# Optimization experiments

Hardware: AMD Instinct MI355X
Metric: run time of the kernel (lower is better)

## Reference

```python
import jax, jax.numpy as jnp
import numpy as np

N_EMBD = 1024
N_HEAD = 16
HEAD_SIZE = N_EMBD // N_HEAD  # 64
ROPE_BASE = 10000.0


def apply_rope(x, pos):
    # x: [B, T, H, D] (torchtune layout), interleaved-pair rotation
    D = x.shape[-1]
    theta = 1.0 / (ROPE_BASE ** (jnp.arange(0, D, 2, dtype=jnp.float32) / D))  # [D/2]
    ang = pos.astype(jnp.float32)[:, None] * theta[None, :]                    # [T, D/2]
    cos = jnp.cos(ang)[None, :, None, :].astype(x.dtype)
    sin = jnp.sin(ang)[None, :, None, :].astype(x.dtype)
    xr = x.reshape(*x.shape[:-1], D // 2, 2)
    x0, x1 = xr[..., 0], xr[..., 1]
    out = jnp.stack([x0 * cos - x1 * sin, x1 * cos + x0 * sin], axis=-1)
    return out.reshape(x.shape)


def setup_inputs() -> dict:
    key = jax.random.key(0)
    k1, k2, k3 = jax.random.split(key, 3)
    B, T = 4, 1000
    x = jax.random.normal(k1, (B, T, N_EMBD), dtype=jnp.float32)
    # causal boolean mask (True = attend), as passed to F.scaled_dot_product_attention
    attn_mask = jnp.tril(jnp.ones((T, T), dtype=bool))[None, None, :, :]
    # Linear weights stored as [in, out] (i.e. torch weight transposed), fan-in scaled
    W_attn = jax.random.normal(k2, (N_EMBD, 3 * N_EMBD), dtype=jnp.float32) * (1.0 / np.sqrt(N_EMBD))
    W_proj = jax.random.normal(k3, (N_EMBD, N_EMBD), dtype=jnp.float32) * (1.0 / np.sqrt(N_EMBD))
    return {"x": x, "attn_mask": attn_mask, "W_attn": W_attn, "W_proj": W_proj}


def reference(x, attn_mask, W_attn, W_proj):
    B, T, C = x.shape
    qkv = x @ W_attn                                   # [B, T, 3C]
    q, k, v = jnp.split(qkv, 3, axis=-1)
    q = q.reshape(B, T, N_HEAD, HEAD_SIZE)
    k = k.reshape(B, T, N_HEAD, HEAD_SIZE)
    v = v.reshape(B, T, N_HEAD, HEAD_SIZE)
    pos = jnp.arange(T)
    q = apply_rope(q, pos)
    k = apply_rope(k, pos)
    # causal SDPA (dropout = 0)
    scale = 1.0 / np.sqrt(HEAD_SIZE)
    scores = jnp.einsum('bqhd,bkhd->bhqk', q, k) * scale   # [B, H, T, T]
    neg = jnp.asarray(jnp.finfo(scores.dtype).min, scores.dtype)
    scores = jnp.where(attn_mask, scores, neg)
    probs = jax.nn.softmax(scores, axis=-1)
    y = jnp.einsum('bhqk,bkhd->bqhd', probs, v)             # [B, T, H, D]
    y = y.reshape(B, T, C)
    return y @ W_proj
```

## Files before the change

### kernel.cpp

```cpp
#include <hip/hip_runtime.h>

typedef unsigned short ushortT;
typedef unsigned int uintT;
typedef __attribute__((ext_vector_type(8))) short bf16x8;
typedef __attribute__((ext_vector_type(4))) float f32x4;

#define B_ 4
#define T_ 1000
#define H_ 16
#define MP 4096
#define QSCALE 0.18033688011112042f

__device__ __forceinline__ ushortT f2bf(float f) {
    unsigned u = __float_as_uint(f);
    u += 0x7fffu + ((u >> 16) & 1u);
    return (ushortT)(u >> 16);
}
__device__ __forceinline__ float fast_exp2(float x) {
#if __has_builtin(__builtin_amdgcn_exp2f)
    return __builtin_amdgcn_exp2f(x);
#else
    return exp2f(x);
#endif
}

__global__ void prep_kernel(const float* __restrict__ x,
                            const float* __restrict__ Wa, const float* __restrict__ Wp,
                            ushortT* __restrict__ Xb,
                            ushortT* __restrict__ Wat, ushortT* __restrict__ Wpt) {
    __shared__ float tile[64][65];
    int bid = blockIdx.x, tid = threadIdx.x;
    if (bid < 4096) {
        int e = (bid * 256 + tid) * 4;
        int r = e >> 10, col = e & 1023;
        int b = r >> 10, t = r & 1023;
        ushort4 o = make_ushort4(0, 0, 0, 0);
        if (t < T_) {
            float4 v = *(const float4*)(x + (((size_t)(b * T_ + t)) << 10) + col);
            o.x = f2bf(v.x); o.y = f2bf(v.y); o.z = f2bf(v.z); o.w = f2bf(v.w);
        }
        *(ushort4*)(Xb + (size_t)e) = o;
        return;
    }
    const float* W; ushortT* Wt; int N, bx, by;
    if (bid < 4096 + 768) { W = Wa; Wt = Wat; N = 3072; int id = bid - 4096; bx = id % 48; by = id / 48; }
    else                  { W = Wp; Wt = Wpt; N = 1024; int id = bid - 4864; bx = id & 15; by = id >> 4; }
    int k0 = by * 64, n0 = bx * 64;
    int lane = tid & 63, w4 = tid >> 6;
#pragma unroll 4
    for (int i = 0; i < 16; ++i) {
        int row = i * 4 + w4;
        tile[row][lane] = W[(size_t)(k0 + row) * N + n0 + lane];
    }
    __syncthreads();
#pragma unroll 4
    for (int i = 0; i < 16; ++i) {
        int row = i * 4 + w4;
        Wt[(size_t)(n0 + row) * 1024 + k0 + lane] = f2bf(tile[lane][row]);
    }
}

__global__ __launch_bounds__(256, 2) void gemm_qkv_kernel(
    const ushortT* __restrict__ A, const ushortT* __restrict__ Bt,
    ushortT* __restrict__ Qb, ushortT* __restrict__ Kb, ushortT* __restrict__ Vtb)
{
    __shared__ __align__(16) ushortT smem[16896];
    ushortT* As = smem;
    ushortT* Bs = smem + 8192;
    const int K = 1024;
    int tid = threadIdx.x, wave = tid >> 6, lane = tid & 63;
    int m0 = blockIdx.y * 128, n0 = blockIdx.x * 128;
    int wm = (wave >> 1) * 64, wn = (wave & 1) * 64;
    int col0 = lane & 15, quad = lane >> 4;

    f32x4 acc[4][4] = {};

    for (int kt = 0; kt < 16; ++kt) {
        int k0 = kt * 64;
        __syncthreads();
#pragma unroll
        for (int it = 0; it < 4; ++it) {
            int gci = (wave * 4 + it) * 64 + lane;
            int r = gci >> 3, c = gci & 7;
            int sc = c ^ (r & 7);
            const ushortT* ga = A + (size_t)(m0 + r) * K + k0 + sc * 8;
            __builtin_amdgcn_global_load_lds(
                (const __attribute__((address_space(1))) unsigned int*)ga,
                (__attribute__((address_space(3))) unsigned int*)(As + (wave * 4 + it) * 512),
                16, 0, 0);
            const ushortT* gb = Bt + (size_t)(n0 + r) * K + k0 + sc * 8;
            __builtin_amdgcn_global_load_lds(
                (const __attribute__((address_space(1))) unsigned int*)gb,
                (__attribute__((address_space(3))) unsigned int*)(Bs + (wave * 4 + it) * 512),
                16, 0, 0);
        }
        __syncthreads();
#pragma unroll
        for (int s = 0; s < 2; ++s) {
            int g = s * 4 + quad;
            bf16x8 af[4], bfr[4];
#pragma unroll
            for (int mi = 0; mi < 4; ++mi) {
                int r = wm + mi * 16 + col0;
                af[mi] = *(const bf16x8*)(As + r * 64 + ((g ^ (r & 7)) * 8));
            }
#pragma unroll
            for (int ni = 0; ni < 4; ++ni) {
                int r = wn + ni * 16 + col0;
                bfr[ni] = *(const bf16x8*)(Bs + r * 64 + ((g ^ (r & 7)) * 8));
            }
#pragma unroll
            for (int mi = 0; mi < 4; ++mi)
#pragma unroll
                for (int ni = 0; ni < 4; ++ni)
                    acc[mi][ni] = __builtin_amdgcn_mfma_f32_16x16x32_bf16(
                        af[mi], bfr[ni], acc[mi][ni], 0, 0, 0);
        }
    }
    __syncthreads();

    int sec = n0 >> 10, cb = n0 & 1023;
    int b = m0 >> 10, tbase = m0 & 1023;

    if (sec < 2) {
        float2* tab = (float2*)smem;
#pragma unroll
        for (int i = 0; i < 16; ++i) {
            int task = i * 256 + tid;
            int tl = task >> 5, p = task & 31;
            float theta = __expf(-(float)p * 0.28782313662425572f);
            float ang = (float)(tbase + tl) * theta;
            float sn, cs;
            sincosf(ang, &sn, &cs);
            tab[tl * 33 + p] = make_float2(cs, sn);
        }
        __syncthreads();
        ushortT* Out = sec ? Kb : Qb;
        float qs = sec ? 1.0f : QSCALE;
#pragma unroll
        for (int mi = 0; mi < 4; ++mi) {
#pragma unroll
            for (int j = 0; j < 4; ++j) {
                int tl = wm + mi * 16 + quad * 4 + j;
                int t = tbase + tl;
                bool valid = t < T_;
#pragma unroll
                for (int nt = 0; nt < 4; ++nt) {
                    float xv = acc[mi][nt][j];
                    float xp = __shfl_xor(xv, 1);
                    int cl = wn + nt * 16 + col0;
                    int d = cl & 63;
                    float2 cssn = tab[tl * 33 + (d >> 1)];
                    float r = (d & 1) ? (xv * cssn.x + xp * cssn.y)
                                      : (xv * cssn.x - xp * cssn.y);
                    r *= qs;
                    if (valid)
                        Out[((size_t)((b << 4) | ((cb + cl) >> 6)) << 16) + (t << 6) + d] = f2bf(r);
                }
            }
        }
    } else {
        ushortT* Ls = smem;
#pragma unroll
        for (int mi = 0; mi < 4; ++mi) {
#pragma unroll
            for (int nt = 0; nt < 4; ++nt) {
                int cl = wn + nt * 16 + col0;
                int rb = wm + mi * 16 + quad * 4;
                uintT lo = (uintT)f2bf(acc[mi][nt][0]) | ((uintT)f2bf(acc[mi][nt][1]) << 16);
                uintT hi = (uintT)f2bf(acc[mi][nt][2]) | ((uintT)f2bf(acc[mi][nt][3]) << 16);
                *(uint2*)(Ls + cl * 132 + rb) = make_uint2(lo, hi);
            }
        }
        __syncthreads();
#pragma unroll
        for (int it = 0; it < 8; ++it) {
            int u = it * 256 + tid;
            int cl = u >> 4, c = u & 15;
            int d = cl & 63, h = (cb + cl) >> 6;
            ushortT tmp[8];
#pragma unroll
            for (int j = 0; j < 8; ++j) tmp[j] = Ls[cl * 132 + j * 16 + c];
            *(bf16x8*)(Vtb + (((size_t)((b << 4) | h)) << 16) + ((size_t)d << 10) + tbase + c * 8)
                = *(bf16x8*)tmp;
        }
    }
}

#define PSTR 136
template <bool LAST>
__device__ __forceinline__ void softmax_store(f32x4* sc4, ushortT* Ps,
                                              int wave, int quad, int col0,
                                              int q0, int j0) {
#pragma unroll
    for (int reg = 0; reg < 4; ++reg) {
        int m = quad * 4 + reg;
        int q = q0 + wave * 16 + m;
        float pv[8];
#pragma unroll
        for (int nt = 0; nt < 8; ++nt) {
            float p = fast_exp2(sc4[nt][reg]);
            if (LAST && (j0 + nt * 16 + col0) > q) p = 0.f;
            pv[nt] = p;
        }
        int4 pk;
        pk.x = __builtin_amdgcn_perm(__float_as_uint(pv[1]), __float_as_uint(pv[0]), 0x07060302u);
        pk.y = __builtin_amdgcn_perm(__float_as_uint(pv[3]), __float_as_uint(pv[2]), 0x07060302u);
        pk.z = __builtin_amdgcn_perm(__float_as_uint(pv[5]), __float_as_uint(pv[4]), 0x07060302u);
        pk.w = __builtin_amdgcn_perm(__float_as_uint(pv[7]), __float_as_uint(pv[6]), 0x07060302u);
        *(int4*)(Ps + (wave * 16 + m) * PSTR + col0 * 8) = pk;
    }
}

__global__ __launch_bounds__(256, 3) void attn_mfma_kernel(
    const ushortT* __restrict__ Qb, const ushortT* __restrict__ Kb,
    const ushortT* __restrict__ Vtb, ushortT* __restrict__ Yb)
{
    __shared__ __align__(16) ushortT Ks[128 * 64];
    __shared__ __align__(16) ushortT Vs[64 * 128];
    __shared__ __align__(16) ushortT Ps[64 * PSTR];

    int flat = blockIdx.y * 64 + blockIdx.x;
    int xcd = flat & 7;
    int slot = flat >> 3;
    int bh = xcd * 8 + (slot & 7);
    int qi = 15 - (slot >> 3);
    int b = bh >> 4, h = bh & 15;
    int q0 = qi * 64;
    int tid = threadIdx.x, wave = tid >> 6, lane = tid & 63;
    int col0 = lane & 15, quad = lane >> 4;

    const ushortT* Kbh  = Kb  + ((size_t)bh << 16);
    const ushortT* Vtbh = Vtb + ((size_t)bh << 16);

    const ushortT* qrowp = Qb + ((size_t)bh << 16) + (size_t)(q0 + wave * 16 + col0) * 64;
    bf16x8 aq[2];
    aq[0] = *(const bf16x8*)(qrowp + quad * 8);
    aq[1] = *(const bf16x8*)(qrowp + 32 + quad * 8);

    bf16x8 onesb;
#pragma unroll
    for (int i = 0; i < 8; ++i) onesb[i] = (short)0x3F80;

    f32x4 o[4] = {};
    f32x4 lsum = {};

    int nchunks = qi / 2 + 1;
    for (int cc = 0; cc < nchunks; ++cc) {
        int j0 = cc * 128;
        __syncthreads();
#pragma unroll
        for (int it = 0; it < 4; ++it) {
            int gci = (wave * 4 + it) * 64 + lane;
            {
                int r = gci >> 3, c = gci & 7;
                int sc = c ^ (r & 7);
                const ushortT* gk = Kbh + (size_t)(j0 + r) * 64 + sc * 8;
                __builtin_amdgcn_global_load_lds(
                    (const __attribute__((address_space(1))) unsigned int*)gk,
                    (__attribute__((address_space(3))) unsigned int*)(Ks + (wave * 4 + it) * 512),
                    16, 0, 0);
            }
            {
                int d = gci >> 4, c = gci & 15;
                int sc = c ^ (d & 15);
                const ushortT* gv = Vtbh + (size_t)d * 1024 + j0 + sc * 8;
                __builtin_amdgcn_global_load_lds(
                    (const __attribute__((address_space(1))) unsigned int*)gv,
                    (__attribute__((address_space(3))) unsigned int*)(Vs + (wave * 4 + it) * 512),
                    16, 0, 0);
            }
        }
        __syncthreads();

        f32x4 sc4[8] = {};
#pragma unroll
        for (int s = 0; s < 2; ++s) {
#pragma unroll
            for (int nt = 0; nt < 8; ++nt) {
                int r = nt * 16 + col0;
                bf16x8 bk = *(const bf16x8*)(Ks + r * 64 + (((s * 4 + quad) ^ (col0 & 7)) * 8));
                sc4[nt] = __builtin_amdgcn_mfma_f32_16x16x32_bf16(aq[s], bk, sc4[nt], 0, 0, 0);
            }
        }

        if (cc == nchunks - 1)
            softmax_store<true>(sc4, Ps, wave, quad, col0, q0, j0);
        else
            softmax_store<false>(sc4, Ps, wave, quad, col0, q0, j0);

#pragma unroll
        for (int s = 0; s < 4; ++s) {
            bf16x8 ap = *(const bf16x8*)(Ps + (wave * 16 + col0) * PSTR + s * 32 + quad * 8);
            lsum = __builtin_amdgcn_mfma_f32_16x16x32_bf16(ap, onesb, lsum, 0, 0, 0);
#pragma unroll
            for (int nt = 0; nt < 4; ++nt) {
                int d = nt * 16 + col0;
                bf16x8 bv = *(const bf16x8*)(Vs + d * 128 + (((s * 4 + quad) ^ col0) * 8));
                o[nt] = __builtin_amdgcn_mfma_f32_16x16x32_bf16(ap, bv, o[nt], 0, 0, 0);
            }
        }
    }

#pragma unroll
    for (int reg = 0; reg < 4; ++reg) {
        int q = q0 + wave * 16 + quad * 4 + reg;
        if (q < T_) {
            float inv_l = 1.0f / lsum[reg];
            ushortT* yp = Yb + ((size_t)(b * 1024 + q) << 10) + h * 64;
#pragma unroll
            for (int nt = 0; nt < 4; ++nt)
                yp[nt * 16 + col0] = f2bf(o[nt][reg] * inv_l);
        }
    }
}

__global__ __launch_bounds__(256, 3) void gemm_proj_kernel(
    const ushortT* __restrict__ A, const ushortT* __restrict__ Bt,
    float* __restrict__ Cout)
{
    __shared__ __align__(16) ushortT As[64 * 64];
    __shared__ __align__(16) ushortT Bs[128 * 64];
    const int K = 1024;
    int tid = threadIdx.x, wave = tid >> 6, lane = tid & 63;
    int m0 = blockIdx.y * 64, n0 = blockIdx.x * 128;
    int wm = (wave >> 1) * 32, wn = (wave & 1) * 64;
    int col0 = lane & 15, quad = lane >> 4;

    f32x4 acc[2][4] = {};

    for (int kt = 0; kt < 16; ++kt) {
        int k0 = kt * 64;
        __syncthreads();
#pragma unroll
        for (int it = 0; it < 2; ++it) {
            int gci = it * 256 + tid;
            int r = gci >> 3, c = gci & 7;
            int sc = c ^ (r & 7);
            const ushortT* ga = A + (size_t)(m0 + r) * K + k0 + sc * 8;
            __builtin_amdgcn_global_load_lds(
                (const __attribute__((address_space(1))) unsigned int*)ga,
                (__attribute__((address_space(3))) unsigned int*)(As + it * 2048 + wave * 512),
                16, 0, 0);
        }
#pragma unroll
        for (int it = 0; it < 4; ++it) {
            int gci = it * 256 + tid;
            int r = gci >> 3, c = gci & 7;
            int sc = c ^ (r & 7);
            const ushortT* gb = Bt + (size_t)(n0 + r) * K + k0 + sc * 8;
            __builtin_amdgcn_global_load_lds(
                (const __attribute__((address_space(1))) unsigned int*)gb,
                (__attribute__((address_space(3))) unsigned int*)(Bs + it * 2048 + wave * 512),
                16, 0, 0);
        }
        __syncthreads();
#pragma unroll
        for (int s = 0; s < 2; ++s) {
            int g = s * 4 + quad;
            bf16x8 af[2], bfr[4];
#pragma unroll
            for (int mi = 0; mi < 2; ++mi) {
                int r = wm + mi * 16 + col0;
                af[mi] = *(const bf16x8*)(As + r * 64 + ((g ^ (r & 7)) * 8));
            }
#pragma unroll
            for (int ni = 0; ni < 4; ++ni) {
                int r = wn + ni * 16 + col0;
                bfr[ni] = *(const bf16x8*)(Bs + r * 64 + ((g ^ (r & 7)) * 8));
            }
#pragma unroll
            for (int mi = 0; mi < 2; ++mi)
#pragma unroll
                for (int ni = 0; ni < 4; ++ni)
                    acc[mi][ni] = __builtin_amdgcn_mfma_f32_16x16x32_bf16(
                        af[mi], bfr[ni], acc[mi][ni], 0, 0, 0);
        }
    }

#pragma unroll
    for (int mi = 0; mi < 2; ++mi) {
#pragma unroll
        for (int j = 0; j < 4; ++j) {
            int row = m0 + wm + mi * 16 + quad * 4 + j;
            int t = row & 1023, b = row >> 10;
            if (t < T_) {
                float* cp = Cout + ((size_t)(b * T_ + t) << 10) + n0 + wn;
#pragma unroll
                for (int ni = 0; ni < 4; ++ni)
                    cp[ni * 16 + col0] = acc[mi][ni][j];
            }
        }
    }
}

extern "C" void kernel_launch(void* const* d_in, const int* in_sizes, int n_in,
                              void* d_out, int out_size, void* d_ws, size_t ws_size,
                              hipStream_t stream) {
    const float* x      = (const float*)d_in[0];
    const float* W_attn = (const float*)d_in[2];
    const float* W_proj = (const float*)d_in[3];
    float* out = (float*)d_out;

    uintptr_t w = (uintptr_t)d_ws;
    ushortT* Xb  = (ushortT*)(w);
    ushortT* Wat = (ushortT*)(w + 8388608);
    ushortT* Wpt = (ushortT*)(w + 14680064);
    ushortT* Qb  = (ushortT*)(w + 16777216);
    ushortT* Kb  = (ushortT*)(w + 25165824);
    ushortT* Vtb = (ushortT*)(w + 33554432);
    ushortT* Yb  = (ushortT*)(w + 41943040);

    prep_kernel<<<dim3(5120), dim3(256), 0, stream>>>(x, W_attn, W_proj, Xb, Wat, Wpt);

    gemm_qkv_kernel<<<dim3(24, 32), dim3(256), 0, stream>>>(Xb, Wat, Qb, Kb, Vtb);

    attn_mfma_kernel<<<dim3(64, 16), dim3(256), 0, stream>>>(Qb, Kb, Vtb, Yb);

    gemm_proj_kernel<<<dim3(8, 64), dim3(256), 0, stream>>>(Yb, Wpt, out);
}
```

Baseline: 151.4 us.

## Split long causal attention tiles across two blocks and combine partials

```diff
diff --git a/kernel.cpp b/kernel.cpp
--- a/kernel.cpp
+++ b/kernel.cpp
@@ -214,19 +214,25 @@
 
 __global__ __launch_bounds__(256, 3) void attn_mfma_kernel(
     const ushortT* __restrict__ Qb, const ushortT* __restrict__ Kb,
-    const ushortT* __restrict__ Vtb, ushortT* __restrict__ Yb)
+    const ushortT* __restrict__ Vtb, ushortT* __restrict__ Yb,
+    float* __restrict__ Opart)
 {
     __shared__ __align__(16) ushortT Ks[128 * 64];
     __shared__ __align__(16) ushortT Vs[64 * 128];
     __shared__ __align__(16) ushortT Ps[64 * PSTR];
 
-    int flat = blockIdx.y * 64 + blockIdx.x;
+    int flat = blockIdx.x;
     int xcd = flat & 7;
     int slot = flat >> 3;
-    int bh = xcd * 8 + (slot & 7);
-    int qi = 15 - (slot >> 3);
+    int bhl = slot & 7;
+    int widx = slot >> 3;
+    int bh = xcd * 8 + bhl;
+    int qi, sp, S;
+    if (widx < 16) { qi = 15 - (widx >> 1); sp = widx & 1; S = 2; }
+    else           { qi = 7 - (widx - 16); sp = 0; S = 1; }
     int b = bh >> 4, h = bh & 15;
     int q0 = qi * 64;
+    int nchunks = qi / 2 + 1;
     int tid = threadIdx.x, wave = tid >> 6, lane = tid & 63;
     int col0 = lane & 15, quad = lane >> 4;
 
@@ -245,8 +251,7 @@
     f32x4 o[4] = {};
     f32x4 lsum = {};
 
-    int nchunks = qi / 2 + 1;
-    for (int cc = 0; cc < nchunks; ++cc) {
+    for (int cc = sp; cc < nchunks; cc += S) {
         int j0 = cc * 128;
         __syncthreads();
 #pragma unroll
@@ -302,17 +307,61 @@
         }
     }
 
-#pragma unroll
-    for (int reg = 0; reg < 4; ++reg) {
-        int q = q0 + wave * 16 + quad * 4 + reg;
-        if (q < T_) {
+    if (S == 1) {
+#pragma unroll
+        for (int reg = 0; reg < 4; ++reg) {
+            int q = q0 + wave * 16 + quad * 4 + reg;
             float inv_l = 1.0f / lsum[reg];
             ushortT* yp = Yb + ((size_t)(b * 1024 + q) << 10) + h * 64;
 #pragma unroll
             for (int nt = 0; nt < 4; ++nt)
                 yp[nt * 16 + col0] = f2bf(o[nt][reg] * inv_l);
         }
-    }
+    } else {
+        int part_id = bh * 16 + (15 - qi) * 2 + sp;
+        float* Op = Opart + (size_t)part_id * 4160;
+#pragma unroll
+        for (int reg = 0; reg < 4; ++reg) {
+            int qr = wave * 16 + quad * 4 + reg;
+#pragma unroll
+            for (int nt = 0; nt < 4; ++nt)
+                Op[qr * 64 + nt * 16 + col0] = o[nt][reg];
+            if (col0 == 0)
+                Op[4096 + qr] = lsum[reg];
+        }
+    }
+}
+
+__global__ __launch_bounds__(256) void combine_kernel(
+    const float* __restrict__ Opart, ushortT* __restrict__ Yb)
+{
+    int flat = blockIdx.x;
+    int xcd = flat & 7;
+    int bhl = (flat >> 3) & 7;
+    int qidx = flat >> 6;
+    int bh = xcd * 8 + bhl;
+    int qi = 15 - qidx;
+    int b = bh >> 4, h = bh & 15;
+    const float* P0 = Opart + (size_t)(bh * 16 + qidx * 2) * 4160;
+    const float* P1 = P0 + 4160;
+    int tid = threadIdx.x;
+    int q = tid >> 2, dg = (tid & 3) * 16;
+    int tg = qi * 64 + q;
+    if (tg >= T_) return;
+    float inv = 1.0f / (P0[4096 + q] + P1[4096 + q]);
+    ushortT outv[16];
+#pragma unroll
+    for (int i = 0; i < 4; ++i) {
+        float4 a = *(const float4*)(P0 + q * 64 + dg + i * 4);
+        float4 c = *(const float4*)(P1 + q * 64 + dg + i * 4);
+        outv[i * 4 + 0] = f2bf((a.x + c.x) * inv);
+        outv[i * 4 + 1] = f2bf((a.y + c.y) * inv);
+        outv[i * 4 + 2] = f2bf((a.z + c.z) * inv);
+        outv[i * 4 + 3] = f2bf((a.w + c.w) * inv);
+    }
+    ushortT* yp = Yb + ((size_t)(b * 1024 + tg) << 10) + h * 64 + dg;
+    *(bf16x8*)yp = *(bf16x8*)outv;
+    *(bf16x8*)(yp + 8) = *(bf16x8*)(outv + 8);
 }
 
 __global__ __launch_bounds__(256, 3) void gemm_proj_kernel(
@@ -403,19 +452,22 @@
     float* out = (float*)d_out;
 
     uintptr_t w = (uintptr_t)d_ws;
-    ushortT* Xb  = (ushortT*)(w);
-    ushortT* Wat = (ushortT*)(w + 8388608);
-    ushortT* Wpt = (ushortT*)(w + 14680064);
-    ushortT* Qb  = (ushortT*)(w + 16777216);
-    ushortT* Kb  = (ushortT*)(w + 25165824);
-    ushortT* Vtb = (ushortT*)(w + 33554432);
-    ushortT* Yb  = (ushortT*)(w + 41943040);
+    ushortT* Xb    = (ushortT*)(w);
+    ushortT* Wat   = (ushortT*)(w + 8388608);
+    ushortT* Wpt   = (ushortT*)(w + 14680064);
+    ushortT* Qb    = (ushortT*)(w + 16777216);
+    ushortT* Kb    = (ushortT*)(w + 25165824);
+    ushortT* Vtb   = (ushortT*)(w + 33554432);
+    ushortT* Yb    = (ushortT*)(w + 41943040);
+    float*   Opart = (float*)(w + 50331648);
 
     prep_kernel<<<dim3(5120), dim3(256), 0, stream>>>(x, W_attn, W_proj, Xb, Wat, Wpt);
 
     gemm_qkv_kernel<<<dim3(24, 32), dim3(256), 0, stream>>>(Xb, Wat, Qb, Kb, Vtb);
 
-    attn_mfma_kernel<<<dim3(64, 16), dim3(256), 0, stream>>>(Qb, Kb, Vtb, Yb);
+    attn_mfma_kernel<<<dim3(1536), dim3(256), 0, stream>>>(Qb, Kb, Vtb, Yb, Opart);
+
+    combine_kernel<<<dim3(512), dim3(256), 0, stream>>>(Opart, Yb);
 
     gemm_proj_kernel<<<dim3(8, 64), dim3(256), 0, stream>>>(Yb, Wpt, out);
 }
```

Result: slower. 161.1 us (+6.5%).

## Double-buffer 64-wide K/V tiles in attention with prefetch of next chunk

Applied to the files above, without the earlier changes.

```diff
diff --git a/kernel.cpp b/kernel.cpp
--- a/kernel.cpp
+++ b/kernel.cpp
@@ -174,50 +174,28 @@
         }
         __syncthreads();
 #pragma unroll
-        for (int it = 0; it < 8; ++it) {
+        for (int it = 0; it < 16; ++it) {
             int u = it * 256 + tid;
-            int cl = u >> 4, c = u & 15;
+            int c4 = u & 15;
+            int g  = (u >> 4) & 1;
+            int cl = u >> 5;
             int d = cl & 63, h = (cb + cl) >> 6;
-            ushortT tmp[8];
-#pragma unroll
-            for (int j = 0; j < 8; ++j) tmp[j] = Ls[cl * 132 + j * 16 + c];
-            *(bf16x8*)(Vtb + (((size_t)((b << 4) | h)) << 16) + ((size_t)d << 10) + tbase + c * 8)
-                = *(bf16x8*)tmp;
-        }
-    }
-}
-
-#define PSTR 136
-template <bool LAST>
-__device__ __forceinline__ void softmax_store(f32x4* sc4, ushortT* Ps,
-                                              int wave, int quad, int col0,
-                                              int q0, int j0) {
-#pragma unroll
-    for (int reg = 0; reg < 4; ++reg) {
-        int m = quad * 4 + reg;
-        int q = q0 + wave * 16 + m;
-        float pv[8];
-#pragma unroll
-        for (int nt = 0; nt < 8; ++nt) {
-            float p = fast_exp2(sc4[nt][reg]);
-            if (LAST && (j0 + nt * 16 + col0) > q) p = 0.f;
-            pv[nt] = p;
-        }
-        int4 pk;
-        pk.x = __builtin_amdgcn_perm(__float_as_uint(pv[1]), __float_as_uint(pv[0]), 0x07060302u);
-        pk.y = __builtin_amdgcn_perm(__float_as_uint(pv[3]), __float_as_uint(pv[2]), 0x07060302u);
-        pk.z = __builtin_amdgcn_perm(__float_as_uint(pv[5]), __float_as_uint(pv[4]), 0x07060302u);
-        pk.w = __builtin_amdgcn_perm(__float_as_uint(pv[7]), __float_as_uint(pv[6]), 0x07060302u);
-        *(int4*)(Ps + (wave * 16 + m) * PSTR + col0 * 8) = pk;
-    }
-}
-
+            ushortT tmp[4];
+#pragma unroll
+            for (int j = 0; j < 4; ++j) tmp[j] = Ls[cl * 132 + g * 64 + j * 16 + c4];
+            *(uint2*)(Vtb + (((size_t)((b << 4) | h)) << 16) + ((size_t)d << 10)
+                      + tbase + g * 64 + c4 * 4) = *(uint2*)tmp;
+        }
+    }
+}
+
+#define PSTR 68
 __global__ __launch_bounds__(256, 3) void attn_mfma_kernel(
     const ushortT* __restrict__ Qb, const ushortT* __restrict__ Kb,
     const ushortT* __restrict__ Vtb, ushortT* __restrict__ Yb)
 {
-    __shared__ __align__(16) ushortT Ks[128 * 64];
-    __shared__ __align__(16) ushortT Vs[64 * 128];
+    __shared__ __align__(16) ushortT Ks[2][64 * 64];
+    __shared__ __align__(16) ushortT Vs[2][64 * 64];
     __shared__ __align__(16) ushortT Ps[64 * PSTR];
 
     int flat = blockIdx.y * 64 + blockIdx.x;
@@ -245,58 +223,75 @@
     f32x4 o[4] = {};
     f32x4 lsum = {};
 
-    int nchunks = qi / 2 + 1;
+    int nchunks = qi + 1;
+
+    auto stage = [&](int cc, ushortT* KsB, ushortT* VsB) {
+#pragma unroll
+        for (int it = 0; it < 2; ++it) {
+            int gci = (wave * 2 + it) * 64 + lane;
+            int r = gci >> 3, c = gci & 7;
+            int sc = c ^ (r & 7);
+            const ushortT* gk = Kbh + (size_t)(cc * 64 + r) * 64 + sc * 8;
+            __builtin_amdgcn_global_load_lds(
+                (const __attribute__((address_space(1))) unsigned int*)gk,
+                (__attribute__((address_space(3))) unsigned int*)(KsB + (wave * 2 + it) * 512),
+                16, 0, 0);
+            const ushortT* gv = Vtbh + (size_t)r * 1024 + cc * 64 + sc * 8;
+            __builtin_amdgcn_global_load_lds(
+                (const __attribute__((address_space(1))) unsigned int*)gv,
+                (__attribute__((address_space(3))) unsigned int*)(VsB + (wave * 2 + it) * 512),
+                16, 0, 0);
+        }
+    };
+
+    stage(0, Ks[0], Vs[0]);
+
     for (int cc = 0; cc < nchunks; ++cc) {
-        int j0 = cc * 128;
-        __syncthreads();
-#pragma unroll
-        for (int it = 0; it < 4; ++it) {
-            int gci = (wave * 4 + it) * 64 + lane;
-            {
-                int r = gci >> 3, c = gci & 7;
-                int sc = c ^ (r & 7);
-                const ushortT* gk = Kbh + (size_t)(j0 + r) * 64 + sc * 8;
-                __builtin_amdgcn_global_load_lds(
-                    (const __attribute__((address_space(1))) unsigned int*)gk,
-                    (__attribute__((address_space(3))) unsigned int*)(Ks + (wave * 4 + it) * 512),
-                    16, 0, 0);
-            }
-            {
-                int d = gci >> 4, c = gci & 15;
-                int sc = c ^ (d & 15);
-                const ushortT* gv = Vtbh + (size_t)d * 1024 + j0 + sc * 8;
-                __builtin_amdgcn_global_load_lds(
-                    (const __attribute__((address_space(1))) unsigned int*)gv,
-                    (__attribute__((address_space(3))) unsigned int*)(Vs + (wave * 4 + it) * 512),
-                    16, 0, 0);
-            }
-        }
-        __syncthreads();
-
-        f32x4 sc4[8] = {};
+        __syncthreads();
+        if (cc + 1 < nchunks)
+            stage(cc + 1, Ks[(cc + 1) & 1], Vs[(cc + 1) & 1]);
+
+        const ushortT* KsC = Ks[cc & 1];
+        const ushortT* VsC = Vs[cc & 1];
+        int j0 = cc * 64;
+
+        f32x4 sc4[4] = {};
 #pragma unroll
         for (int s = 0; s < 2; ++s) {
 #pragma unroll
-            for (int nt = 0; nt < 8; ++nt) {
+            for (int nt = 0; nt < 4; ++nt) {
                 int r = nt * 16 + col0;
-                bf16x8 bk = *(const bf16x8*)(Ks + r * 64 + (((s * 4 + quad) ^ (col0 & 7)) * 8));
+                bf16x8 bk = *(const bf16x8*)(KsC + r * 64 + (((s * 4 + quad) ^ (r & 7)) * 8));
                 sc4[nt] = __builtin_amdgcn_mfma_f32_16x16x32_bf16(aq[s], bk, sc4[nt], 0, 0, 0);
             }
         }
 
-        if (cc == nchunks - 1)
-            softmax_store<true>(sc4, Ps, wave, quad, col0, q0, j0);
-        else
-            softmax_store<false>(sc4, Ps, wave, quad, col0, q0, j0);
-
-#pragma unroll
-        for (int s = 0; s < 4; ++s) {
+        bool last = (cc == nchunks - 1);
+#pragma unroll
+        for (int reg = 0; reg < 4; ++reg) {
+            int m = quad * 4 + reg;
+            int q = q0 + wave * 16 + m;
+            float pv[4];
+#pragma unroll
+            for (int nt = 0; nt < 4; ++nt) {
+                float p = fast_exp2(sc4[nt][reg]);
+                if (last && (j0 + nt * 16 + col0) > q) p = 0.f;
+                pv[nt] = p;
+            }
+            uint2 pk;
+            pk.x = __builtin_amdgcn_perm(__float_as_uint(pv[1]), __float_as_uint(pv[0]), 0x07060302u);
+            pk.y = __builtin_amdgcn_perm(__float_as_uint(pv[3]), __float_as_uint(pv[2]), 0x07060302u);
+            *(uint2*)(Ps + (wave * 16 + m) * PSTR + col0 * 4) = pk;
+        }
+
+#pragma unroll
+        for (int s = 0; s < 2; ++s) {
             bf16x8 ap = *(const bf16x8*)(Ps + (wave * 16 + col0) * PSTR + s * 32 + quad * 8);
             lsum = __builtin_amdgcn_mfma_f32_16x16x32_bf16(ap, onesb, lsum, 0, 0, 0);
 #pragma unroll
             for (int nt = 0; nt < 4; ++nt) {
                 int d = nt * 16 + col0;
-                bf16x8 bv = *(const bf16x8*)(Vs + d * 128 + (((s * 4 + quad) ^ col0) * 8));
+                bf16x8 bv = *(const bf16x8*)(VsC + d * 64 + (((s * 4 + quad) ^ (d & 7)) * 8));
                 o[nt] = __builtin_amdgcn_mfma_f32_16x16x32_bf16(ap, bv, o[nt], 0, 0, 0);
             }
         }
```

Measured after the change: 156.0 us. 1.03x slower.

## Fuse prep, QKV GEMM, attention and projection into one cooperative persistent kernel

Applied to the files above, without the earlier changes.

```diff
diff --git a/kernel.cpp b/kernel.cpp
--- a/kernel.cpp
+++ b/kernel.cpp
@@ -1,15 +1,16 @@
 #include <hip/hip_runtime.h>
+#include <hip/hip_cooperative_groups.h>
+
+namespace cg = cooperative_groups;
 
 typedef unsigned short ushortT;
 typedef unsigned int uintT;
 typedef __attribute__((ext_vector_type(8))) short bf16x8;
 typedef __attribute__((ext_vector_type(4))) float f32x4;
 
-#define B_ 4
 #define T_ 1000
-#define H_ 16
-#define MP 4096
 #define QSCALE 0.18033688011112042f
+#define PSTR 136
 
 __device__ __forceinline__ ushortT f2bf(float f) {
     unsigned u = __float_as_uint(f);
@@ -24,382 +25,377 @@
 #endif
 }
 
-__global__ void prep_kernel(const float* __restrict__ x,
-                            const float* __restrict__ Wa, const float* __restrict__ Wp,
-                            ushortT* __restrict__ Xb,
-                            ushortT* __restrict__ Wat, ushortT* __restrict__ Wpt) {
-    __shared__ float tile[64][65];
-    int bid = blockIdx.x, tid = threadIdx.x;
-    if (bid < 4096) {
-        int e = (bid * 256 + tid) * 4;
-        int r = e >> 10, col = e & 1023;
-        int b = r >> 10, t = r & 1023;
-        ushort4 o = make_ushort4(0, 0, 0, 0);
-        if (t < T_) {
-            float4 v = *(const float4*)(x + (((size_t)(b * T_ + t)) << 10) + col);
-            o.x = f2bf(v.x); o.y = f2bf(v.y); o.z = f2bf(v.z); o.w = f2bf(v.w);
-        }
-        *(ushort4*)(Xb + (size_t)e) = o;
-        return;
-    }
-    const float* W; ushortT* Wt; int N, bx, by;
-    if (bid < 4096 + 768) { W = Wa; Wt = Wat; N = 3072; int id = bid - 4096; bx = id % 48; by = id / 48; }
-    else                  { W = Wp; Wt = Wpt; N = 1024; int id = bid - 4864; bx = id & 15; by = id >> 4; }
-    int k0 = by * 64, n0 = bx * 64;
-    int lane = tid & 63, w4 = tid >> 6;
+__global__ __launch_bounds__(256, 3) void fused_kernel(
+    const float* __restrict__ x, const float* __restrict__ Wa, const float* __restrict__ Wp,
+    ushortT* __restrict__ Xb, ushortT* __restrict__ Wat, ushortT* __restrict__ Wpt,
+    ushortT* __restrict__ Qb, ushortT* __restrict__ Kb, ushortT* __restrict__ Vtb,
+    ushortT* __restrict__ Yb, float* __restrict__ out)
+{
+    __shared__ __align__(16) ushortT smem[25088];
+    cg::grid_group grid = cg::this_grid();
+    int blk = blockIdx.x, nb = gridDim.x, tid = threadIdx.x;
+    int wave = tid >> 6, lane = tid & 63;
+    int col0 = lane & 15, quad = lane >> 4;
+
+    {
+        float (*tile)[65] = (float(*)[65])smem;
+        for (int u = blk; u < 5120; u += nb) {
+            if (u < 4096) {
+                int e = (u * 256 + tid) * 4;
+                int r = e >> 10, col = e & 1023;
+                int b = r >> 10, t = r & 1023;
+                ushort4 o = make_ushort4(0, 0, 0, 0);
+                if (t < T_) {
+                    float4 v = *(const float4*)(x + (((size_t)(b * T_ + t)) << 10) + col);
+                    o.x = f2bf(v.x); o.y = f2bf(v.y); o.z = f2bf(v.z); o.w = f2bf(v.w);
+                }
+                *(ushort4*)(Xb + (size_t)e) = o;
+            } else {
+                const float* W; ushortT* Wt; int N, bx, by;
+                int id = u - 4096;
+                if (id < 768) { W = Wa; Wt = Wat; N = 3072; bx = id % 48; by = id / 48; }
+                else          { W = Wp; Wt = Wpt; N = 1024; id -= 768; bx = id & 15; by = id >> 4; }
+                int k0 = by * 64, n0 = bx * 64;
+                int w4 = tid >> 6;
+                __syncthreads();
 #pragma unroll 4
-    for (int i = 0; i < 16; ++i) {
-        int row = i * 4 + w4;
-        tile[row][lane] = W[(size_t)(k0 + row) * N + n0 + lane];
-    }
-    __syncthreads();
+                for (int i = 0; i < 16; ++i) {
+                    int row = i * 4 + w4;
+                    tile[row][lane] = W[(size_t)(k0 + row) * N + n0 + lane];
+                }
+                __syncthreads();
 #pragma unroll 4
-    for (int i = 0; i < 16; ++i) {
-        int row = i * 4 + w4;
-        Wt[(size_t)(n0 + row) * 1024 + k0 + lane] = f2bf(tile[lane][row]);
-    }
-}
-
-__global__ __launch_bounds__(256, 2) void gemm_qkv_kernel(
-    const ushortT* __restrict__ A, const ushortT* __restrict__ Bt,
-    ushortT* __restrict__ Qb, ushortT* __restrict__ Kb, ushortT* __restrict__ Vtb)
-{
-    __shared__ __align__(16) ushortT smem[16896];
-    ushortT* As = smem;
-    ushortT* Bs = smem + 8192;
-    const int K = 1024;
-    int tid = threadIdx.x, wave = tid >> 6, lane = tid & 63;
-    int m0 = blockIdx.y * 128, n0 = blockIdx.x * 128;
-    int wm = (wave >> 1) * 64, wn = (wave & 1) * 64;
-    int col0 = lane & 15, quad = lane >> 4;
-
-    f32x4 acc[4][4] = {};
-
-    for (int kt = 0; kt < 16; ++kt) {
-        int k0 = kt * 64;
-        __syncthreads();
-#pragma unroll
-        for (int it = 0; it < 4; ++it) {
-            int gci = (wave * 4 + it) * 64 + lane;
-            int r = gci >> 3, c = gci & 7;
-            int sc = c ^ (r & 7);
-            const ushortT* ga = A + (size_t)(m0 + r) * K + k0 + sc * 8;
-            __builtin_amdgcn_global_load_lds(
-                (const __attribute__((address_space(1))) unsigned int*)ga,
-                (__attribute__((address_space(3))) unsigned int*)(As + (wave * 4 + it) * 512),
-                16, 0, 0);
-            const ushortT* gb = Bt + (size_t)(n0 + r) * K + k0 + sc * 8;
-            __builtin_amdgcn_global_load_lds(
-                (const __attribute__((address_space(1))) unsigned int*)gb,
-                (__attribute__((address_space(3))) unsigned int*)(Bs + (wave * 4 + it) * 512),
-                16, 0, 0);
-        }
-        __syncthreads();
-#pragma unroll
-        for (int s = 0; s < 2; ++s) {
-            int g = s * 4 + quad;
-            bf16x8 af[4], bfr[4];
-#pragma unroll
-            for (int mi = 0; mi < 4; ++mi) {
-                int r = wm + mi * 16 + col0;
-                af[mi] = *(const bf16x8*)(As + r * 64 + ((g ^ (r & 7)) * 8));
-            }
-#pragma unroll
-            for (int ni = 0; ni < 4; ++ni) {
-                int r = wn + ni * 16 + col0;
-                bfr[ni] = *(const bf16x8*)(Bs + r * 64 + ((g ^ (r & 7)) * 8));
-            }
-#pragma unroll
-            for (int mi = 0; mi < 4; ++mi)
-#pragma unroll
-                for (int ni = 0; ni < 4; ++ni)
-                    acc[mi][ni] = __builtin_amdgcn_mfma_f32_16x16x32_bf16(
-                        af[mi], bfr[ni], acc[mi][ni], 0, 0, 0);
+                for (int i = 0; i < 16; ++i) {
+                    int row = i * 4 + w4;
+                    Wt[(size_t)(n0 + row) * 1024 + k0 + lane] = f2bf(tile[lane][row]);
+                }
+            }
         }
     }
-    __syncthreads();
-
-    int sec = n0 >> 10, cb = n0 & 1023;
-    int b = m0 >> 10, tbase = m0 & 1023;
-
-    if (sec < 2) {
-        float2* tab = (float2*)smem;
-#pragma unroll
-        for (int i = 0; i < 16; ++i) {
-            int task = i * 256 + tid;
-            int tl = task >> 5, p = task & 31;
-            float theta = __expf(-(float)p * 0.28782313662425572f);
-            float ang = (float)(tbase + tl) * theta;
-            float sn, cs;
-            sincosf(ang, &sn, &cs);
-            tab[tl * 33 + p] = make_float2(cs, sn);
+    grid.sync();
+
+    {
+        ushortT* As = smem;
+        ushortT* Bs = smem + 8192;
+        const int K = 1024;
+        for (int tix = blk; tix < 768; tix += nb) {
+            int m0 = (tix / 24) * 128, n0 = (tix % 24) * 128;
+            int wm = (wave >> 1) * 64, wn = (wave & 1) * 64;
+
+            f32x4 acc[4][4] = {};
+
+            for (int kt = 0; kt < 16; ++kt) {
+                int k0 = kt * 64;
+                __syncthreads();
+#pragma unroll
+                for (int it = 0; it < 4; ++it) {
+                    int gci = (wave * 4 + it) * 64 + lane;
+                    int r = gci >> 3, c = gci & 7;
+                    int sc = c ^ (r & 7);
+                    const ushortT* ga = Xb + (size_t)(m0 + r) * K + k0 + sc * 8;
+                    __builtin_amdgcn_global_load_lds(
+                        (const __attribute__((address_space(1))) unsigned int*)ga,
+                        (__attribute__((address_space(3))) unsigned int*)(As + (wave * 4 + it) * 512),
+                        16, 0, 0);
+                    const ushortT* gb = Wat + (size_t)(n0 + r) * K + k0 + sc * 8;
+                    __builtin_amdgcn_global_load_lds(
+                        (const __attribute__((address_space(1))) unsigned int*)gb,
+                        (__attribute__((address_space(3))) unsigned int*)(Bs + (wave * 4 + it) * 512),
+                        16, 0, 0);
+                }
+                __syncthreads();
+#pragma unroll
+                for (int s = 0; s < 2; ++s) {
+                    int g = s * 4 + quad;
+                    bf16x8 af[4], bfr[4];
+#pragma unroll
+                    for (int mi = 0; mi < 4; ++mi) {
+                        int r = wm + mi * 16 + col0;
+                        af[mi] = *(const bf16x8*)(As + r * 64 + ((g ^ (r & 7)) * 8));
+                    }
+#pragma unroll
+                    for (int ni = 0; ni < 4; ++ni) {
+                        int r = wn + ni * 16 + col0;
+                        bfr[ni] = *(const bf16x8*)(Bs + r * 64 + ((g ^ (r & 7)) * 8));
+                    }
+#pragma unroll
+                    for (int mi = 0; mi < 4; ++mi)
+#pragma unroll
+                        for (int ni = 0; ni < 4; ++ni)
+                            acc[mi][ni] = __builtin_amdgcn_mfma_f32_16x16x32_bf16(
+                                af[mi], bfr[ni], acc[mi][ni], 0, 0, 0);
+                }
+            }
+            __syncthreads();
+
+            int sec = n0 >> 10, cb = n0 & 1023;
+            int b = m0 >> 10, tbase = m0 & 1023;
+
+            if (sec < 2) {
+                float2* tab = (float2*)smem;
+#pragma unroll
+                for (int i = 0; i < 16; ++i) {
+                    int task = i * 256 + tid;
+                    int tl = task >> 5, p = task & 31;
+                    float theta = __expf(-(float)p * 0.28782313662425572f);
+                    float ang = (float)(tbase + tl) * theta;
+                    float sn, cs;
+                    sincosf(ang, &sn, &cs);
+                    tab[tl * 33 + p] = make_float2(cs, sn);
+                }
+                __syncthreads();
+                ushortT* Out = sec ? Kb : Qb;
+                float qs = sec ? 1.0f : QSCALE;
+#pragma unroll
+                for (int mi = 0; mi < 4; ++mi) {
+#pragma unroll
+                    for (int j = 0; j < 4; ++j) {
+                        int tl = wm + mi * 16 + quad * 4 + j;
+                        int t = tbase + tl;
+                        bool valid = t < T_;
+#pragma unroll
+                        for (int nt = 0; nt < 4; ++nt) {
+                            float xv = acc[mi][nt][j];
+                            float xp = __shfl_xor(xv, 1);
+                            int cl = wn + nt * 16 + col0;
+                            int d = cl & 63;
+                            float2 cssn = tab[tl * 33 + (d >> 1)];
+                            float r = (d & 1) ? (xv * cssn.x + xp * cssn.y)
+                                              : (xv * cssn.x - xp * cssn.y);
+                            r *= qs;
+                            if (valid)
+                                Out[((size_t)((b << 4) | ((cb + cl) >> 6)) << 16) + (t << 6) + d] = f2bf(r);
+                        }
+                    }
+                }
+            } else {
+                ushortT* Ls = smem;
+#pragma unroll
+                for (int mi = 0; mi < 4; ++mi) {
+#pragma unroll
+                    for (int nt = 0; nt < 4; ++nt) {
+                        int cl = wn + nt * 16 + col0;
+                        int rb = wm + mi * 16 + quad * 4;
+                        uintT lo = (uintT)f2bf(acc[mi][nt][0]) | ((uintT)f2bf(acc[mi][nt][1]) << 16);
+                        uintT hi = (uintT)f2bf(acc[mi][nt][2]) | ((uintT)f2bf(acc[mi][nt][3]) << 16);
+                        *(uint2*)(Ls + cl * 132 + rb) = make_uint2(lo, hi);
+                    }
+                }
+                __syncthreads();
+#pragma unroll
+                for (int it = 0; it < 8; ++it) {
+                    int u = it * 256 + tid;
+                    int cl = u >> 4, c = u & 15;
+                    int d = cl & 63, h = (cb + cl) >> 6;
+                    ushortT tmp[8];
+#pragma unroll
+                    for (int j = 0; j < 8; ++j) tmp[j] = Ls[cl * 132 + j * 16 + c];
+                    *(bf16x8*)(Vtb + (((size_t)((b << 4) | h)) << 16) + ((size_t)d << 10) + tbase + c * 8)
+                        = *(bf16x8*)tmp;
+                }
+            }
         }
-        __syncthreads();
-        ushortT* Out = sec ? Kb : Qb;
-        float qs = sec ? 1.0f : QSCALE;
-#pragma unroll
-        for (int mi = 0; mi < 4; ++mi) {
-#pragma unroll
-            for (int j = 0; j < 4; ++j) {
-                int tl = wm + mi * 16 + quad * 4 + j;
-                int t = tbase + tl;
-                bool valid = t < T_;
-#pragma unroll
-                for (int nt = 0; nt < 4; ++nt) {
-                    float xv = acc[mi][nt][j];
-                    float xp = __shfl_xor(xv, 1);
-                    int cl = wn + nt * 16 + col0;
-                    int d = cl & 63;
-                    float2 cssn = tab[tl * 33 + (d >> 1)];
-                    float r = (d & 1) ? (xv * cssn.x + xp * cssn.y)
-                                      : (xv * cssn.x - xp * cssn.y);
-                    r *= qs;
-                    if (valid)
-                        Out[((size_t)((b << 4) | ((cb + cl) >> 6)) << 16) + (t << 6) + d] = f2bf(r);
+    }
+    grid.sync();
+
+    {
+        ushortT* Ks = smem;
+        ushortT* Vs = smem + 8192;
+        ushortT* Ps = smem + 16384;
+        for (int w = blk; w < 1024; w += nb) {
+            int xcd = w & 7;
+            int slot = w >> 3;
+            int bh = xcd * 8 + (slot & 7);
+            int qi = 15 - (slot >> 3);
+            int b = bh >> 4, h = bh & 15;
+            int q0 = qi * 64;
+
+            const ushortT* Kbh  = Kb  + ((size_t)bh << 16);
+            const ushortT* Vtbh = Vtb + ((size_t)bh << 16);
+
+            const ushortT* qrowp = Qb + ((size_t)bh << 16) + (size_t)(q0 + wave * 16 + col0) * 64;
+            bf16x8 aq[2];
+            aq[0] = *(const bf16x8*)(qrowp + quad * 8);
+            aq[1] = *(const bf16x8*)(qrowp + 32 + quad * 8);
+
+            bf16x8 onesb;
+#pragma unroll
+            for (int i = 0; i < 8; ++i) onesb[i] = (short)0x3F80;
+
+            f32x4 o[4] = {};
+            f32x4 lsum = {};
+
+            int nchunks = qi / 2 + 1;
+            for (int cc = 0; cc < nchunks; ++cc) {
+                int j0 = cc * 128;
+                __syncthreads();
+#pragma unroll
+                for (int it = 0; it < 4; ++it) {
+                    int gci = (wave * 4 + it) * 64 + lane;
+                    {
+                        int r = gci >> 3, c = gci & 7;
+                        int sc = c ^ (r & 7);
+                        const ushortT* gk = Kbh + (size_t)(j0 + r) * 64 + sc * 8;
+                        __builtin_amdgcn_global_load_lds(
+                            (const __attribute__((address_space(1))) unsigned int*)gk,
+                            (__attribute__((address_space(3))) unsigned int*)(Ks + (wave * 4 + it) * 512),
+                            16, 0, 0);
+                    }
+                    {
+                        int d = gci >> 4, c = gci & 15;
+                        int sc = c ^ (d & 15);
+                        const ushortT* gv = Vtbh + (size_t)d * 1024 + j0 + sc * 8;
+                        __builtin_amdgcn_global_load_lds(
+                            (const __attribute__((address_space(1))) unsigned int*)gv,
+                            (__attribute__((address_space(3))) unsigned int*)(Vs + (wave * 4 + it) * 512),
+                            16, 0, 0);
+                    }
+                }
+                __syncthreads();
+
+                f32x4 sc4[8] = {};
+#pragma unroll
+                for (int s = 0; s < 2; ++s) {
+#pragma unroll
+                    for (int nt = 0; nt < 8; ++nt) {
+                        int r = nt * 16 + col0;
+                        bf16x8 bk = *(const bf16x8*)(Ks + r * 64 + (((s * 4 + quad) ^ (col0 & 7)) * 8));
+                        sc4[nt] = __builtin_amdgcn_mfma_f32_16x16x32_bf16(aq[s], bk, sc4[nt], 0, 0, 0);
+                    }
+                }
+
+                bool last = (cc == nchunks - 1);
+#pragma unroll
+                for (int reg = 0; reg < 4; ++reg) {
+                    int m = quad * 4 + reg;
+                    int q = q0 + wave * 16 + m;
+                    float pv[8];
+#pragma unroll
+                    for (int nt = 0; nt < 8; ++nt) {
+                        float p = fast_exp2(sc4[nt][reg]);
+                        if (last && (j0 + nt * 16 + col0) > q) p = 0.f;
+                        pv[nt] = p;
+                    }
+                    int4 pk;
+                    pk.x = __builtin_amdgcn_perm(__float_as_uint(pv[1]), __float_as_uint(pv[0]), 0x07060302u);
+                    pk.y = __builtin_amdgcn_perm(__float_as_uint(pv[3]), __float_as_uint(pv[2]), 0x07060302u);
+                    pk.z = __builtin_amdgcn_perm(__float_as_uint(pv[5]), __float_as_uint(pv[4]), 0x07060302u);
+                    pk.w = __builtin_amdgcn_perm(__float_as_uint(pv[7]), __float_as_uint(pv[6]), 0x07060302u);
+                    *(int4*)(Ps + (wave * 16 + m) * PSTR + col0 * 8) = pk;
+                }
+
+#pragma unroll
+                for (int s = 0; s < 4; ++s) {
+                    bf16x8 ap = *(const bf16x8*)(Ps + (wave * 16 + col0) * PSTR + s * 32 + quad * 8);
+                    lsum = __builtin_amdgcn_mfma_f32_16x16x32_bf16(ap, onesb, lsum, 0, 0, 0);
+#pragma unroll
+                    for (int nt = 0; nt < 4; ++nt) {
+                        int d = nt * 16 + col0;
+                        bf16x8 bv = *(const bf16x8*)(Vs + d * 128 + (((s * 4 + quad) ^ col0) * 8));
+                        o[nt] = __builtin_amdgcn_mfma_f32_16x16x32_bf16(ap, bv, o[nt], 0, 0, 0);
+                    }
+                }
+            }
+
+#pragma unroll
+            for (int reg = 0; reg < 4; ++reg) {
+                int q = q0 + wave * 16 + quad * 4 + reg;
+                if (q < T_) {
+                    float inv_l = 1.0f / lsum[reg];
+                    ushortT* yp = Yb + ((size_t)(b * 1024 + q) << 10) + h * 64;
+#pragma unroll
+                    for (int nt = 0; nt < 4; ++nt)
+                        yp[nt * 16 + col0] = f2bf(o[nt][reg] * inv_l);
                 }
             }
         }
-    } else {
-        ushortT* Ls = smem;
-#pragma unroll
-        for (int mi = 0; mi < 4; ++mi) {
-#pragma unroll
-            for (int nt = 0; nt < 4; ++nt) {
-                int cl = wn + nt * 16 + col0;
-                int rb = wm + mi * 16 + quad * 4;
-                uintT lo = (uintT)f2bf(acc[mi][nt][0]) | ((uintT)f2bf(acc[mi][nt][1]) << 16);
-                uintT hi = (uintT)f2bf(acc[mi][nt][2]) | ((uintT)f2bf(acc[mi][nt][3]) << 16);
-                *(uint2*)(Ls + cl * 132 + rb) = make_uint2(lo, hi);
-            }
-        }
-        __syncthreads();
-#pragma unroll
-        for (int it = 0; it < 8; ++it) {
-            int u = it * 256 + tid;
-            int cl = u >> 4, c = u & 15;
-            int d = cl & 63, h = (cb + cl) >> 6;
-            ushortT tmp[8];
-#pragma unroll
-            for (int j = 0; j < 8; ++j) tmp[j] = Ls[cl * 132 + j * 16 + c];
-            *(bf16x8*)(Vtb + (((size_t)((b << 4) | h)) << 16) + ((size_t)d << 10) + tbase + c * 8)
-                = *(bf16x8*)tmp;
+    }
+    grid.sync();
+
+    {
+        ushortT* As = smem;
+        ushortT* Bs = smem + 4096;
+        const int K = 1024;
+        for (int w = blk; w < 512; w += nb) {
+            int m0 = (w >> 3) * 64, n0 = (w & 7) * 128;
+            int wm = (wave >> 1) * 32, wn = (wave & 1) * 64;
+
+            f32x4 acc[2][4] = {};
+
+            for (int kt = 0; kt < 16; ++kt) {
+                int k0 = kt * 64;
+                __syncthreads();
+#pragma unroll
+                for (int it = 0; it < 2; ++it) {
+                    int gci = it * 256 + tid;
+                    int r = gci >> 3, c = gci & 7;
+                    int sc = c ^ (r & 7);
+                    const ushortT* ga = Yb + (size_t)(m0 + r) * K + k0 + sc * 8;
+                    __builtin_amdgcn_global_load_lds(
+                        (const __attribute__((address_space(1))) unsigned int*)ga,
+                        (__attribute__((address_space(3))) unsigned int*)(As + it * 2048 + wave * 512),
+                        16, 0, 0);
+                }
+#pragma unroll
+                for (int it = 0; it < 4; ++it) {
+                    int gci = it * 256 + tid;
+                    int r = gci >> 3, c = gci & 7;
+                    int sc = c ^ (r & 7);
+                    const ushortT* gb = Wpt + (size_t)(n0 + r) * K + k0 + sc * 8;
+                    __builtin_amdgcn_global_load_lds(
+                        (const __attribute__((address_space(1))) unsigned int*)gb,
+                        (__attribute__((address_space(3))) unsigned int*)(Bs + it * 2048 + wave * 512),
+                        16, 0, 0);
+                }
+                __syncthreads();
+#pragma unroll
+                for (int s = 0; s < 2; ++s) {
+                    int g = s * 4 + quad;
+                    bf16x8 af[2], bfr[4];
+#pragma unroll
+                    for (int mi = 0; mi < 2; ++mi) {
+                        int r = wm + mi * 16 + col0;
+                        af[mi] = *(const bf16x8*)(As + r * 64 + ((g ^ (r & 7)) * 8));
+                    }
+#pragma unroll
+                    for (int ni = 0; ni < 4; ++ni) {
+                        int r = wn + ni * 16 + col0;
+                        bfr[ni] = *(const bf16x8*)(Bs + r * 64 + ((g ^ (r & 7)) * 8));
+                    }
+#pragma unroll
+                    for (int mi = 0; mi < 2; ++mi)
+#pragma unroll
+                        for (int ni = 0; ni < 4; ++ni)
+                            acc[mi][ni] = __builtin_amdgcn_mfma_f32_16x16x32_bf16(
+                                af[mi], bfr[ni], acc[mi][ni], 0, 0, 0);
+                }
+            }
+            __syncthreads();
+
+#pragma unroll
+            for (int mi = 0; mi < 2; ++mi) {
+#pragma unroll
+                for (int j = 0; j < 4; ++j) {
+                    int row = m0 + wm + mi * 16 + quad * 4 + j;
+                    int t = row & 1023, b = row >> 10;
+                    if (t < T_) {
+                        float* cp = out + ((size_t)(b * T_ + t) << 10) + n0 + wn;
+#pragma unroll
+                        for (int ni = 0; ni < 4; ++ni)
+                            cp[ni * 16 + col0] = acc[mi][ni][j];
+                    }
+                }
+            }
         }
     }
 }
 
-#define PSTR 136
-template <bool LAST>
-__device__ __forceinline__ void softmax_store(f32x4* sc4, ushortT* Ps,
-                                              int wave, int quad, int col0,
-                                              int q0, int j0) {
-#pragma unroll
-    for (int reg = 0; reg < 4; ++reg) {
-        int m = quad * 4 + reg;
-        int q = q0 + wave * 16 + m;
-        float pv[8];
-#pragma unroll
-        for (int nt = 0; nt < 8; ++nt) {
-            float p = fast_exp2(sc4[nt][reg]);
-            if (LAST && (j0 + nt * 16 + col0) > q) p = 0.f;
-            pv[nt] = p;
-        }
-        int4 pk;
-        pk.x = __builtin_amdgcn_perm(__float_as_uint(pv[1]), __float_as_uint(pv[0]), 0x07060302u);
-        pk.y = __builtin_amdgcn_perm(__float_as_uint(pv[3]), __float_as_uint(pv[2]), 0x07060302u);
-        pk.z = __builtin_amdgcn_perm(__float_as_uint(pv[5]), __float_as_uint(pv[4]), 0x07060302u);
-        pk.w = __builtin_amdgcn_perm(__float_as_uint(pv[7]), __float_as_uint(pv[6]), 0x07060302u);
-        *(int4*)(Ps + (wave * 16 + m) * PSTR + col0 * 8) = pk;
-    }
-}
-
-__global__ __launch_bounds__(256, 3) void attn_mfma_kernel(
-    const ushortT* __restrict__ Qb, const ushortT* __restrict__ Kb,
-    const ushortT* __restrict__ Vtb, ushortT* __restrict__ Yb)
-{
-    __shared__ __align__(16) ushortT Ks[128 * 64];
-    __shared__ __align__(16) ushortT Vs[64 * 128];
-    __shared__ __align__(16) ushortT Ps[64 * PSTR];
-
-    int flat = blockIdx.y * 64 + blockIdx.x;
-    int xcd = flat & 7;
-    int slot = flat >> 3;
-    int bh = xcd * 8 + (slot & 7);
-    int qi = 15 - (slot >> 3);
-    int b = bh >> 4, h = bh & 15;
-    int q0 = qi * 64;
-    int tid = threadIdx.x, wave = tid >> 6, lane = tid & 63;
-    int col0 = lane & 15, quad = lane >> 4;
-
-    const ushortT* Kbh  = Kb  + ((size_t)bh << 16);
-    const ushortT* Vtbh = Vtb + ((size_t)bh << 16);
-
-    const ushortT* qrowp = Qb + ((size_t)bh << 16) + (size_t)(q0 + wave * 16 + col0) * 64;
-    bf16x8 aq[2];
-    aq[0] = *(const bf16x8*)(qrowp + quad * 8);
-    aq[1] = *(const bf16x8*)(qrowp + 32 + quad * 8);
-
-    bf16x8 onesb;
-#pragma unroll
-    for (int i = 0; i < 8; ++i) onesb[i] = (short)0x3F80;
-
-    f32x4 o[4] = {};
-    f32x4 lsum = {};
-
-    int nchunks = qi / 2 + 1;
-    for (int cc = 0; cc < nchunks; ++cc) {
-        int j0 = cc * 128;
-        __syncthreads();
-#pragma unroll
-        for (int it = 0; it < 4; ++it) {
-            int gci = (wave * 4 + it) * 64 + lane;
-            {
-                int r = gci >> 3, c = gci & 7;
-                int sc = c ^ (r & 7);
-                const ushortT* gk = Kbh + (size_t)(j0 + r) * 64 + sc * 8;
-                __builtin_amdgcn_global_load_lds(
-                    (const __attribute__((address_space(1))) unsigned int*)gk,
-                    (__attribute__((address_space(3))) unsigned int*)(Ks + (wave * 4 + it) * 512),
-                    16, 0, 0);
-            }
-            {
-                int d = gci >> 4, c = gci & 15;
-                int sc = c ^ (d & 15);
-                const ushortT* gv = Vtbh + (size_t)d * 1024 + j0 + sc * 8;
-                __builtin_amdgcn_global_load_lds(
-                    (const __attribute__((address_space(1))) unsigned int*)gv,
-                    (__attribute__((address_space(3))) unsigned int*)(Vs + (wave * 4 + it) * 512),
-                    16, 0, 0);
-            }
-        }
-        __syncthreads();
-
-        f32x4 sc4[8] = {};
-#pragma unroll
-        for (int s = 0; s < 2; ++s) {
-#pragma unroll
-            for (int nt = 0; nt < 8; ++nt) {
-                int r = nt * 16 + col0;
-                bf16x8 bk = *(const bf16x8*)(Ks + r * 64 + (((s * 4 + quad) ^ (col0 & 7)) * 8));
-                sc4[nt] = __builtin_amdgcn_mfma_f32_16x16x32_bf16(aq[s], bk, sc4[nt], 0, 0, 0);
-            }
-        }
-
-        if (cc == nchunks - 1)
-            softmax_store<true>(sc4, Ps, wave, quad, col0, q0, j0);
-        else
-            softmax_store<false>(sc4, Ps, wave, quad, col0, q0, j0);
-
-#pragma unroll
-        for (int s = 0; s < 4; ++s) {
-            bf16x8 ap = *(const bf16x8*)(Ps + (wave * 16 + col0) * PSTR + s * 32 + quad * 8);
-            lsum = __builtin_amdgcn_mfma_f32_16x16x32_bf16(ap, onesb, lsum, 0, 0, 0);
-#pragma unroll
-            for (int nt = 0; nt < 4; ++nt) {
-                int d = nt * 16 + col0;
-                bf16x8 bv = *(const bf16x8*)(Vs + d * 128 + (((s * 4 + quad) ^ col0) * 8));
-                o[nt] = __builtin_amdgcn_mfma_f32_16x16x32_bf16(ap, bv, o[nt], 0, 0, 0);
-            }
-        }
-    }
-
-#pragma unroll
-    for (int reg = 0; reg < 4; ++reg) {
-        int q = q0 + wave * 16 + quad * 4 + reg;
-        if (q < T_) {
-            float inv_l = 1.0f / lsum[reg];
-            ushortT* yp = Yb + ((size_t)(b * 1024 + q) << 10) + h * 64;
-#pragma unroll
-            for (int nt = 0; nt < 4; ++nt)
-                yp[nt * 16 + col0] = f2bf(o[nt][reg] * inv_l);
-        }
-    }
-}
-
-__global__ __launch_bounds__(256, 3) void gemm_proj_kernel(
-    const ushortT* __restrict__ A, const ushortT* __restrict__ Bt,
-    float* __restrict__ Cout)
-{
-    __shared__ __align__(16) ushortT As[64 * 64];
-    __shared__ __align__(16) ushortT Bs[128 * 64];
-    const int K = 1024;
-    int tid = threadIdx.x, wave = tid >> 6, lane = tid & 63;
-    int m0 = blockIdx.y * 64, n0 = blockIdx.x * 128;
-    int wm = (wave >> 1) * 32, wn = (wave & 1) * 64;
-    int col0 = lane & 15, quad = lane >> 4;
-
-    f32x4 acc[2][4] = {};
-
-    for (int kt = 0; kt < 16; ++kt) {
-        int k0 = kt * 64;
-        __syncthreads();
-#pragma unroll
-        for (int it = 0; it < 2; ++it) {
-            int gci = it * 256 + tid;
-            int r = gci >> 3, c = gci & 7;
-            int sc = c ^ (r & 7);
-            const ushortT* ga = A + (size_t)(m0 + r) * K + k0 + sc * 8;
-            __builtin_amdgcn_global_load_lds(
-                (const __attribute__((address_space(1))) unsigned int*)ga,
-                (__attribute__((address_space(3))) unsigned int*)(As + it * 2048 + wave * 512),
-                16, 0, 0);
-        }
-#pragma unroll
-        for (int it = 0; it < 4; ++it) {
-            int gci = it * 256 + tid;
-            int r = gci >> 3, c = gci & 7;
-            int sc = c ^ (r & 7);
-            const ushortT* gb = Bt + (size_t)(n0 + r) * K + k0 + sc * 8;
-            __builtin_amdgcn_global_load_lds(
-                (const __attribute__((address_space(1))) unsigned int*)gb,
-                (__attribute__((address_space(3))) unsigned int*)(Bs + it * 2048 + wave * 512),
-                16, 0, 0);
-        }
-        __syncthreads();
-#pragma unroll
-        for (int s = 0; s < 2; ++s) {
-            int g = s * 4 + quad;
-            bf16x8 af[2], bfr[4];
-#pragma unroll
-            for (int mi = 0; mi < 2; ++mi) {
-                int r = wm + mi * 16 + col0;
-                af[mi] = *(const bf16x8*)(As + r * 64 + ((g ^ (r & 7)) * 8));
-            }
-#pragma unroll
-            for (int ni = 0; ni < 4; ++ni) {
-                int r = wn + ni * 16 + col0;
-                bfr[ni] = *(const bf16x8*)(Bs + r * 64 + ((g ^ (r & 7)) * 8));
-            }
-#pragma unroll
-            for (int mi = 0; mi < 2; ++mi)
-#pragma unroll
-                for (int ni = 0; ni < 4; ++ni)
-                    acc[mi][ni] = __builtin_amdgcn_mfma_f32_16x16x32_bf16(
-                        af[mi], bfr[ni], acc[mi][ni], 0, 0, 0);
-        }
-    }
-
-#pragma unroll
-    for (int mi = 0; mi < 2; ++mi) {
-#pragma unroll
-        for (int j = 0; j < 4; ++j) {
-            int row = m0 + wm + mi * 16 + quad * 4 + j;
-            int t = row & 1023, b = row >> 10;
-            if (t < T_) {
-                float* cp = Cout + ((size_t)(b * T_ + t) << 10) + n0 + wn;
-#pragma unroll
-                for (int ni = 0; ni < 4; ++ni)
-                    cp[ni * 16 + col0] = acc[mi][ni][j];
-            }
-        }
-    }
-}
-
 extern "C" void kernel_launch(void* const* d_in, const int* in_sizes, int n_in,
                               void* d_out, int out_size, void* d_ws, size_t ws_size,
                               hipStream_t stream) {
-    const float* x      = (const float*)d_in[0];
-    const float* W_attn = (const float*)d_in[2];
-    const float* W_proj = (const float*)d_in[3];
+    const float* x  = (const float*)d_in[0];
+    const float* Wa = (const float*)d_in[2];
+    const float* Wp = (const float*)d_in[3];
     float* out = (float*)d_out;
 
     uintptr_t w = (uintptr_t)d_ws;
@@ -411,11 +407,17 @@
     ushortT* Vtb = (ushortT*)(w + 33554432);
     ushortT* Yb  = (ushortT*)(w + 41943040);
 
-    prep_kernel<<<dim3(5120), dim3(256), 0, stream>>>(x, W_attn, W_proj, Xb, Wat, Wpt);
-
-    gemm_qkv_kernel<<<dim3(24, 32), dim3(256), 0, stream>>>(Xb, Wat, Qb, Kb, Vtb);
-
-    attn_mfma_kernel<<<dim3(64, 16), dim3(256), 0, stream>>>(Qb, Kb, Vtb, Yb);
-
-    gemm_proj_kernel<<<dim3(8, 64), dim3(256), 0, stream>>>(Yb, Wpt, out);
+    int maxPerCU = 0;
+    if (hipOccupancyMaxActiveBlocksPerMultiprocessor(&maxPerCU, fused_kernel, 256, 0)
+            != hipSuccess || maxPerCU < 1)
+        maxPerCU = 2;
+    int grid = maxPerCU * 256;
+    if (grid > 768) grid = 768;
+
+    void* args[] = { (void*)&x, (void*)&Wa, (void*)&Wp,
+                     (void*)&Xb, (void*)&Wat, (void*)&Wpt,
+                     (void*)&Qb, (void*)&Kb, (void*)&Vtb,
+                     (void*)&Yb, (void*)&out };
+    hipLaunchCooperativeKernel((void*)fused_kernel, dim3(grid), dim3(256),
+                               args, 0, stream);
 }
```

New measurement: 362.8 us. 2.4x slower.
